# Kernel tuning notes

Measured on AMD Instinct MI355X. Metric: run time of the kernel, lower is better.

## Reference

```python
import jax, jax.numpy as jnp
import numpy as np

C = 256
NUM_GROUPS = 32
EPS = 1e-5


def group_norm(x, gamma, beta):
    # x: [B, C, H, W]; normalize within each of NUM_GROUPS channel groups
    B, Cc, H, W = x.shape
    xg = x.reshape(B, NUM_GROUPS, Cc // NUM_GROUPS, H, W)
    mean = xg.mean(axis=(2, 3, 4), keepdims=True)
    var = xg.var(axis=(2, 3, 4), keepdims=True)
    xg = (xg - mean) * jax.lax.rsqrt(var + EPS)
    x = xg.reshape(B, Cc, H, W)
    return x * gamma[None, :, None, None] + beta[None, :, None, None]


def conv1x1(x, w, b):
    # w: [C_out, C_in], b: [C_out]; equivalent to nn.Conv2d(k=1)
    return jnp.einsum('oc,bchw->bohw', w, x) + b[None, :, None, None]


def setup_inputs() -> dict:
    key = jax.random.key(0)
    ks = jax.random.split(key, 12)
    B, H, W = 8, 64, 64
    x = jax.random.normal(ks[0], (B, C, H, W), dtype=jnp.float32)
    temb = jax.random.normal(ks[1], (B, 512), dtype=jnp.float32)
    s = 1.0 / np.sqrt(C)  # kaiming-uniform-ish scale for 1x1 conv
    def wmat(k):
        return jax.random.uniform(k, (C, C), dtype=jnp.float32, minval=-s, maxval=s)
    def bvec(k):
        return jax.random.uniform(k, (C,), dtype=jnp.float32, minval=-s, maxval=s)
    return {
        'x': x, 'temb': temb,
        'gn_w': jnp.ones((C,), jnp.float32), 'gn_b': jnp.zeros((C,), jnp.float32),
        'wq': wmat(ks[2]), 'bq': bvec(ks[3]),
        'wk': wmat(ks[4]), 'bk': bvec(ks[5]),
        'wv': wmat(ks[6]), 'bv': bvec(ks[7]),
        'wp': wmat(ks[8]), 'bp': bvec(ks[9]),
    }


def reference(x, temb, gn_w, gn_b, wq, bq, wk, bk, wv, bv, wp, bp):
    B, Cc, H, W = x.shape
    h = group_norm(x, gn_w, gn_b)
    q = conv1x1(h, wq, bq)
    k = conv1x1(h, wk, bk)
    v = conv1x1(h, wv, bv)
    # full self-attention over spatial positions: scores [B, H, W, H, W]
    scale = Cc ** (-0.5)
    w = jnp.einsum('bchw,bcij->bhwij', q, k) * scale
    w = jax.nn.softmax(w.reshape(B, H, W, H * W), axis=-1).reshape(B, H, W, H, W)
    h = jnp.einsum('bhwij,bcij->bchw', w, v)
    h = conv1x1(h, wp, bp)
    return (x + h, temb)
```

## Files before the change

kernel.cpp:

```cpp
#include <hip/hip_runtime.h>
#include <hip/hip_bf16.h>

#define B_ 8
#define C_ 256
#define S_ 4096
#define G_ 32
#define GC_ 8
#define EPS_ 1e-5f

typedef __attribute__((ext_vector_type(4))) float f32x4;
typedef __attribute__((ext_vector_type(8))) short bf16x8;
typedef __attribute__((ext_vector_type(4))) short bf16x4;
typedef __attribute__((ext_vector_type(4))) unsigned int u32x4;
typedef __attribute__((ext_vector_type(2))) unsigned int u32x2;

#define DI __device__ __forceinline__

DI unsigned short f2bf(float f) {
    union { float f; unsigned u; } v; v.f = f;
    unsigned r = v.u + 0x7fffu + ((v.u >> 16) & 1u);
    return (unsigned short)(r >> 16);
}

DI unsigned cvt_pk_bf16(float lo, float hi) {
    unsigned r;
    asm("v_cvt_pk_bf16_f32 %0, %1, %2" : "=v"(r) : "v"(lo), "v"(hi));
    return r;
}

__global__ __launch_bounds__(256) void k_gn_stats(const float* __restrict__ x,
                                                  float* __restrict__ stats) {
    int bg = blockIdx.x;
    const float4* xp = (const float4*)(x + (size_t)bg * (GC_ * S_));
    float s = 0.f, ss = 0.f;
    for (int i = threadIdx.x; i < GC_ * S_ / 4; i += 256) {
        float4 v = xp[i];
        s  += v.x + v.y + v.z + v.w;
        ss += v.x * v.x + v.y * v.y + v.z * v.z + v.w * v.w;
    }
    #pragma unroll
    for (int off = 32; off; off >>= 1) { s += __shfl_down(s, off); ss += __shfl_down(ss, off); }
    __shared__ float rs[4], rss[4];
    int w = threadIdx.x >> 6;
    if ((threadIdx.x & 63) == 0) { rs[w] = s; rss[w] = ss; }
    __syncthreads();
    if (threadIdx.x == 0) {
        float S1 = rs[0] + rs[1] + rs[2] + rs[3];
        float S2 = rss[0] + rss[1] + rss[2] + rss[3];
        float inv = 1.f / (GC_ * S_);
        float mean = S1 * inv;
        float var = S2 * inv - mean * mean;
        stats[bg * 2] = mean;
        stats[bg * 2 + 1] = rsqrtf(var + EPS_);
    }
}

__global__ __launch_bounds__(256) void k_gn_apply(const float* __restrict__ x,
                                                  const float* __restrict__ stats,
                                                  const float* __restrict__ gw,
                                                  const float* __restrict__ gb,
                                                  unsigned short* __restrict__ h) {
    int b = blockIdx.x >> 6;
    int s0 = (blockIdx.x & 63) * 64;
    __shared__ unsigned short tile[64 * 256];
    const float* xb = x + (size_t)b * C_ * S_;
    for (int id = threadIdx.x; id < 256 * 16; id += 256) {
        int c = id >> 4, s4 = id & 15;
        float4 v = *(const float4*)(xb + (size_t)c * S_ + s0 + s4 * 4);
        float mean = stats[(b * G_ + (c >> 3)) * 2];
        float rstd = stats[(b * G_ + (c >> 3)) * 2 + 1];
        float ga = gw[c], be = gb[c];
        float vv[4] = {v.x, v.y, v.z, v.w};
        #pragma unroll
        for (int i = 0; i < 4; i++) {
            int srow = s4 * 4 + i;
            unsigned byte = srow * 512u + c * 2u;
            byte ^= ((srow & 7u) << 4);
            *(unsigned short*)((char*)tile + byte) = f2bf((vv[i] - mean) * rstd * ga + be);
        }
    }
    __syncthreads();
    unsigned short* hb = h + (size_t)b * S_ * C_;
    for (int id = threadIdx.x; id < 2048; id += 256) {
        int srow = id >> 5, ck = id & 31;
        unsigned byte = srow * 512u + ck * 16u;
        byte ^= ((srow & 7u) << 4);
        u32x4 v = *(u32x4*)((char*)tile + byte);
        *(u32x4*)(hb + (size_t)(s0 + srow) * C_ + ck * 8) = v;
    }
}

__global__ __launch_bounds__(256) void k_wcvt(const float* __restrict__ wq, const float* __restrict__ wk,
                                              const float* __restrict__ wv, const float* __restrict__ wp,
                                              unsigned short* __restrict__ wbf) {
    int t = blockIdx.x * 256 + threadIdx.x;
    int mat = t >> 13;
    int idx = (t & 8191) * 8;
    const float* src = mat == 0 ? wq : mat == 1 ? wk : mat == 2 ? wv : wp;
    float4 a = *(const float4*)(src + idx);
    float4 c = *(const float4*)(src + idx + 4);
    unsigned short tmp[8] = {f2bf(a.x), f2bf(a.y), f2bf(a.z), f2bf(a.w),
                             f2bf(c.x), f2bf(c.y), f2bf(c.z), f2bf(c.w)};
    *(u32x4*)(wbf + mat * 65536 + idx) = *(u32x4*)tmp;
}

__global__ __launch_bounds__(256) void k_qkv(const unsigned short* __restrict__ wbf,
                                             const float* __restrict__ bq,
                                             const float* __restrict__ bk,
                                             const float* __restrict__ bv,
                                             const unsigned short* __restrict__ h,
                                             unsigned short* __restrict__ q_sc,
                                             unsigned short* __restrict__ k_sc,
                                             unsigned short* __restrict__ v_cs,
                                             float qscale) {
    int mode = blockIdx.x >> 9;
    int inner = blockIdx.x & 511;
    int b = inner & 7;
    int rest = inner >> 3;
    int m0 = (rest & 1) * 128;
    int n0 = (rest >> 1) * 128;
    const unsigned short* W = wbf + mode * 65536;
    const float* bias = mode == 0 ? bq : (mode == 1 ? bk : bv);

    __shared__ unsigned short Alds[128 * 64];
    __shared__ unsigned short Blds[128 * 64];
    int tid = threadIdx.x;
    int lane = tid & 63, wv = tid >> 6;
    int wm = (wv >> 1) * 64, wn = (wv & 1) * 64;
    int lr = lane & 15, lg = lane >> 4;
    f32x4 acc[4][4] = {};
    const unsigned short* Bb = h + (size_t)b * S_ * C_;

    for (int k0 = 0; k0 < 256; k0 += 64) {
        __syncthreads();
        #pragma unroll
        for (int i = 0; i < 4; i++) {
            int id = tid + i * 256;
            int row = id >> 3, ck = id & 7;
            u32x4 v = *(const u32x4*)(W + (size_t)(m0 + row) * C_ + k0 + ck * 8);
            unsigned byte = row * 128u + ck * 16u;
            byte ^= ((row & 7u) << 4);
            *(u32x4*)((char*)Alds + byte) = v;
        }
        #pragma unroll
        for (int i = 0; i < 4; i++) {
            int id = tid + i * 256;
            int row = id >> 3, ck = id & 7;
            u32x4 v = *(const u32x4*)(Bb + (size_t)(n0 + row) * C_ + k0 + ck * 8);
            unsigned byte = row * 128u + ck * 16u;
            byte ^= ((row & 7u) << 4);
            *(u32x4*)((char*)Blds + byte) = v;
        }
        __syncthreads();
        #pragma unroll
        for (int ks = 0; ks < 2; ks++) {
            bf16x8 af[4], bf[4];
            #pragma unroll
            for (int mf = 0; mf < 4; mf++) {
                int m = wm + mf * 16 + lr;
                unsigned byte = m * 128u + ks * 64u + lg * 16u;
                byte ^= ((m & 7u) << 4);
                af[mf] = *(bf16x8*)((char*)Alds + byte);
            }
            #pragma unroll
            for (int nf = 0; nf < 4; nf++) {
                int n = wn + nf * 16 + lr;
                unsigned byte = n * 128u + ks * 64u + lg * 16u;
                byte ^= ((n & 7u) << 4);
                bf[nf] = *(bf16x8*)((char*)Blds + byte);
            }
            #pragma unroll
            for (int mf = 0; mf < 4; mf++)
                #pragma unroll
                for (int nf = 0; nf < 4; nf++)
                    acc[mf][nf] = __builtin_amdgcn_mfma_f32_16x16x32_bf16(af[mf], bf[nf], acc[mf][nf], 0, 0, 0);
        }
    }

    if (mode < 2) {
        unsigned short* ob = (mode == 0 ? q_sc : k_sc) + (size_t)b * S_ * C_;
        float sc = mode == 0 ? qscale : 1.f;
        #pragma unroll
        for (int mf = 0; mf < 4; mf++)
            #pragma unroll
            for (int nf = 0; nf < 4; nf++) {
                int cbase = m0 + wm + mf * 16 + lg * 4;
                int srow = n0 + wn + nf * 16 + lr;
                bf16x4 pk;
                #pragma unroll
                for (int r = 0; r < 4; r++)
                    pk[r] = (short)f2bf((acc[mf][nf][r] + bias[cbase + r]) * sc);
                *(bf16x4*)(ob + (size_t)srow * C_ + cbase) = pk;
            }
    } else {
        unsigned short* ob = v_cs + (size_t)b * C_ * S_;
        #pragma unroll
        for (int mf = 0; mf < 4; mf++)
            #pragma unroll
            for (int nf = 0; nf < 4; nf++)
                #pragma unroll
                for (int r = 0; r < 4; r++) {
                    int c = m0 + wm + mf * 16 + lg * 4 + r;
                    int s = n0 + wn + nf * 16 + lr;
                    ob[(size_t)c * S_ + s] = f2bf(acc[mf][nf][r] + bias[c]);
                }
    }
}

__global__ __launch_bounds__(256) void k_proj(const unsigned short* __restrict__ wbf,
                                              const float* __restrict__ bias,
                                              const unsigned short* __restrict__ Bm,
                                              float* __restrict__ outf,
                                              const float* __restrict__ xres) {
    int b = blockIdx.x & 7;
    int rest = blockIdx.x >> 3;
    int m0 = (rest & 1) * 128;
    int n0 = (rest >> 1) * 128;
    const unsigned short* W = wbf + 3 * 65536;

    __shared__ unsigned short Alds[128 * 64];
    __shared__ unsigned short Blds[128 * 64];
    int tid = threadIdx.x;
    int lane = tid & 63, wv = tid >> 6;
    int wm = (wv >> 1) * 64, wn = (wv & 1) * 64;
    int lr = lane & 15, lg = lane >> 4;
    f32x4 acc[4][4] = {};
    const unsigned short* Bb = Bm + (size_t)b * S_ * C_;

    for (int k0 = 0; k0 < 256; k0 += 64) {
        __syncthreads();
        #pragma unroll
        for (int i = 0; i < 4; i++) {
            int id = tid + i * 256;
            int row = id >> 3, ck = id & 7;
            u32x4 v = *(const u32x4*)(W + (size_t)(m0 + row) * C_ + k0 + ck * 8);
            unsigned byte = row * 128u + ck * 16u;
            byte ^= ((row & 7u) << 4);
            *(u32x4*)((char*)Alds + byte) = v;
        }
        #pragma unroll
        for (int i = 0; i < 4; i++) {
            int id = tid + i * 256;
            int row = id >> 3, ck = id & 7;
            u32x4 v = *(const u32x4*)(Bb + (size_t)(n0 + row) * C_ + k0 + ck * 8);
            unsigned byte = row * 128u + ck * 16u;
            byte ^= ((row & 7u) << 4);
            *(u32x4*)((char*)Blds + byte) = v;
        }
        __syncthreads();
        #pragma unroll
        for (int ks = 0; ks < 2; ks++) {
            bf16x8 af[4], bf[4];
            #pragma unroll
            for (int mf = 0; mf < 4; mf++) {
                int m = wm + mf * 16 + lr;
                unsigned byte = m * 128u + ks * 64u + lg * 16u;
                byte ^= ((m & 7u) << 4);
                af[mf] = *(bf16x8*)((char*)Alds + byte);
            }
            #pragma unroll
            for (int nf = 0; nf < 4; nf++) {
                int n = wn + nf * 16 + lr;
                unsigned byte = n * 128u + ks * 64u + lg * 16u;
                byte ^= ((n & 7u) << 4);
                bf[nf] = *(bf16x8*)((char*)Blds + byte);
            }
            #pragma unroll
            for (int mf = 0; mf < 4; mf++)
                #pragma unroll
                for (int nf = 0; nf < 4; nf++)
                    acc[mf][nf] = __builtin_amdgcn_mfma_f32_16x16x32_bf16(af[mf], bf[nf], acc[mf][nf], 0, 0, 0);
        }
    }

    const float* xb = xres + (size_t)b * C_ * S_;
    #pragma unroll
    for (int mf = 0; mf < 4; mf++)
        #pragma unroll
        for (int nf = 0; nf < 4; nf++)
            #pragma unroll
            for (int r = 0; r < 4; r++) {
                int c = m0 + wm + mf * 16 + lg * 4 + r;
                int s = n0 + wn + nf * 16 + lr;
                outf[(size_t)b * C_ * S_ + (size_t)c * S_ + s] =
                    acc[mf][nf][r] + bias[c] + xb[(size_t)c * S_ + s];
            }
}

__global__ __launch_bounds__(512, 2) void k_attn(const unsigned short* __restrict__ Q,
                                                 const unsigned short* __restrict__ K,
                                                 const unsigned short* __restrict__ V,
                                                 unsigned short* __restrict__ O) {
    int b = blockIdx.x & 7;
    int q0 = (blockIdx.x >> 3) * 128;
    int tid = threadIdx.x, lane = tid & 63, wv = tid >> 6;
    int lr = lane & 15, lg = lane >> 4;
    int qg = wv & 3, kg = wv >> 2;
    int qw = q0 + qg * 32;
    __shared__ unsigned short Klds[64 * 256];
    __shared__ unsigned short Vlds[256 * 64];
    __shared__ unsigned short Plds[4][32 * 64];
    __shared__ float mlp[8 * 2 * 16];
    const unsigned short* Qb = Q + (size_t)b * S_ * C_;
    const unsigned short* Kb = K + (size_t)b * S_ * C_;
    const unsigned short* Vb = V + (size_t)b * C_ * S_;

    bf16x8 qf_[8][2];
    #pragma unroll
    for (int ks = 0; ks < 8; ks++)
        #pragma unroll
        for (int qf = 0; qf < 2; qf++)
            qf_[ks][qf] = *(const bf16x8*)(Qb + (size_t)(qw + qf * 16 + lr) * C_ + ks * 32 + lg * 8);

    unsigned kaddr[2][8];
    #pragma unroll
    for (int kf = 0; kf < 2; kf++) {
        int key = kg * 32 + kf * 16 + lr;
        #pragma unroll
        for (int ks = 0; ks < 8; ks++)
            kaddr[kf][ks] = (unsigned)key * 512u + (((unsigned)(4 * ks + lg + 2 * key) & 31u) << 4);
    }

    f32x4 acc[8][2] = {};
    float lrun[2] = {0.f, 0.f};

    int krow[4], kck[4], vc[4], vck[4];
    #pragma unroll
    for (int i = 0; i < 4; i++) {
        int id = tid + i * 512;
        krow[i] = id >> 5; kck[i] = id & 31;
        vc[i] = id >> 3;  vck[i] = id & 7;
    }
    unsigned kwb[4], vwb[4];
    #pragma unroll
    for (int i = 0; i < 4; i++) {
        kwb[i] = krow[i] * 512u + (((unsigned)(kck[i] + 2 * krow[i]) & 31u) << 4);
        vwb[i] = vc[i] * 128u + ((vck[i] * 16u) ^ ((vc[i] & 7u) << 4));
    }

    u32x4 kpre[4], vpre[4];
    #pragma unroll
    for (int i = 0; i < 4; i++) {
        kpre[i] = *(const u32x4*)(Kb + (size_t)krow[i] * C_ + kck[i] * 8);
        vpre[i] = *(const u32x4*)(Vb + (size_t)vc[i] * S_ + vck[i] * 8);
    }
    #pragma unroll
    for (int i = 0; i < 4; i++) {
        *(u32x4*)((char*)Klds + kwb[i]) = kpre[i];
        *(u32x4*)((char*)Vlds + vwb[i]) = vpre[i];
    }
    __syncthreads();

    for (int kt = 0; kt < 64; kt++) {
        bool pf = (kt + 1) < 64;
        if (pf) {
            #pragma unroll
            for (int i = 0; i < 4; i++)
                kpre[i] = *(const u32x4*)(Kb + (size_t)((kt + 1) * 64 + krow[i]) * C_ + kck[i] * 8);
        }

        f32x4 sc[2][2] = {};
        #pragma unroll
        for (int ks = 0; ks < 8; ks++) {
            bf16x8 a[2];
            a[0] = *(const bf16x8*)((char*)Klds + kaddr[0][ks]);
            a[1] = *(const bf16x8*)((char*)Klds + kaddr[1][ks]);
            #pragma unroll
            for (int kf = 0; kf < 2; kf++)
                #pragma unroll
                for (int qf = 0; qf < 2; qf++)
                    sc[kf][qf] = __builtin_amdgcn_mfma_f32_16x16x32_bf16(a[kf], qf_[ks][qf], sc[kf][qf], 0, 0, 0);
        }

        #pragma unroll
        for (int qf = 0; qf < 2; qf++)
            #pragma unroll
            for (int kf = 0; kf < 2; kf++) {
                float p0 = __builtin_amdgcn_exp2f(sc[kf][qf][0] - 16.f);
                float p1 = __builtin_amdgcn_exp2f(sc[kf][qf][1] - 16.f);
                float p2 = __builtin_amdgcn_exp2f(sc[kf][qf][2] - 16.f);
                float p3 = __builtin_amdgcn_exp2f(sc[kf][qf][3] - 16.f);
                lrun[qf] += (p0 + p1) + (p2 + p3);
                u32x2 pk;
                pk[0] = cvt_pk_bf16(p0, p1);
                pk[1] = cvt_pk_bf16(p2, p3);
                int q = qf * 16 + lr;
                unsigned byte = (unsigned)q * 128u + (kg * 32u + kf * 16u + lg * 4u) * 2u;
                byte ^= ((q & 7u) << 4);
                *(u32x2*)((char*)&Plds[qg][0] + byte) = pk;
            }

        if (pf) {
            #pragma unroll
            for (int i = 0; i < 4; i++)
                vpre[i] = *(const u32x4*)(Vb + (size_t)vc[i] * S_ + (kt + 1) * 64 + vck[i] * 8);
        }

        __syncthreads();

        if (pf) {
            #pragma unroll
            for (int i = 0; i < 4; i++)
                *(u32x4*)((char*)Klds + kwb[i]) = kpre[i];
        }

        #pragma unroll
        for (int ks2 = 0; ks2 < 2; ks2++) {
            bf16x8 pb[2];
            #pragma unroll
            for (int qf = 0; qf < 2; qf++) {
                int q = qf * 16 + lr;
                unsigned pbyte = (unsigned)q * 128u + ks2 * 64u + lg * 16u;
                pbyte ^= ((q & 7u) << 4);
                pb[qf] = *(const bf16x8*)((char*)&Plds[qg][0] + pbyte);
            }
            #pragma unroll
            for (int cf = 0; cf < 8; cf++) {
                int c = kg * 128 + cf * 16 + lr;
                unsigned byte = c * 128u + ks2 * 64u + lg * 16u;
                byte ^= ((c & 7u) << 4);
                bf16x8 va = *(const bf16x8*)((char*)Vlds + byte);
                #pragma unroll
                for (int qf = 0; qf < 2; qf++)
                    acc[cf][qf] = __builtin_amdgcn_mfma_f32_16x16x32_bf16(va, pb[qf], acc[cf][qf], 0, 0, 0);
            }
        }

        __syncthreads();

        if (pf) {
            #pragma unroll
            for (int i = 0; i < 4; i++)
                *(u32x4*)((char*)Vlds + vwb[i]) = vpre[i];
        }
    }

    float ls[2];
    #pragma unroll
    for (int qf = 0; qf < 2; qf++) {
        float t = lrun[qf];
        t += __shfl_xor(t, 16);
        t += __shfl_xor(t, 32);
        ls[qf] = t;
    }
    if (lg == 0) {
        #pragma unroll
        for (int qf = 0; qf < 2; qf++) mlp[(wv * 2 + qf) * 16 + lr] = ls[qf];
    }
    __syncthreads();
    unsigned short* Ob = O + (size_t)b * S_ * C_;
    #pragma unroll
    for (int qf = 0; qf < 2; qf++) {
        float inv = 1.f / (ls[qf] + mlp[((wv ^ 4) * 2 + qf) * 16 + lr]);
        int srow = qw + qf * 16 + lr;
        #pragma unroll
        for (int cf = 0; cf < 8; cf++) {
            u32x2 pk;
            pk[0] = cvt_pk_bf16(acc[cf][qf][0] * inv, acc[cf][qf][1] * inv);
            pk[1] = cvt_pk_bf16(acc[cf][qf][2] * inv, acc[cf][qf][3] * inv);
            *(u32x2*)(Ob + (size_t)srow * C_ + kg * 128 + cf * 16 + lg * 4) = pk;
        }
    }
}

__global__ __launch_bounds__(256) void k_copy_temb(const float* __restrict__ t, float* __restrict__ o) {
    int i = blockIdx.x * 256 + threadIdx.x;
    if (i < B_ * 512) o[i] = t[i];
}

extern "C" void kernel_launch(void* const* d_in, const int* in_sizes, int n_in,
                              void* d_out, int out_size, void* d_ws, size_t ws_size,
                              hipStream_t stream) {
    (void)in_sizes; (void)n_in; (void)out_size; (void)ws_size;
    const float* x  = (const float*)d_in[0];
    const float* temb = (const float*)d_in[1];
    const float* gw = (const float*)d_in[2];
    const float* gb = (const float*)d_in[3];
    const float* wq = (const float*)d_in[4];
    const float* bq = (const float*)d_in[5];
    const float* wk = (const float*)d_in[6];
    const float* bk = (const float*)d_in[7];
    const float* wv = (const float*)d_in[8];
    const float* bv = (const float*)d_in[9];
    const float* wp = (const float*)d_in[10];
    const float* bp = (const float*)d_in[11];
    float* out = (float*)d_out;

    char* ws = (char*)d_ws;
    const size_t MB16 = (size_t)B_ * S_ * C_ * 2;
    unsigned short* h_sc = (unsigned short*)ws;
    unsigned short* q_sc = (unsigned short*)(ws + MB16);
    unsigned short* k_sc = (unsigned short*)(ws + 2 * MB16);
    unsigned short* v_cs = (unsigned short*)(ws + 3 * MB16);
    float* stats = (float*)(ws + 4 * MB16);
    unsigned short* wbf = (unsigned short*)(ws + 4 * MB16 + 4096);

    const float qscale = 0.0625f * 1.4426950408889634f;

    k_wcvt<<<128, 256, 0, stream>>>(wq, wk, wv, wp, wbf);
    k_gn_stats<<<B_ * G_, 256, 0, stream>>>(x, stats);
    k_gn_apply<<<B_ * (S_ / 64), 256, 0, stream>>>(x, stats, gw, gb, h_sc);
    k_qkv<<<1536, 256, 0, stream>>>(wbf, bq, bk, bv, h_sc, q_sc, k_sc, v_cs, qscale);
    k_attn<<<B_ * (S_ / 128), 512, 0, stream>>>(q_sc, k_sc, v_cs, h_sc);
    k_proj<<<512, 256, 0, stream>>>(wbf, bp, h_sc, out, x);
    k_copy_temb<<<(B_ * 512 + 255) / 256, 256, 0, stream>>>(temb, out + (size_t)B_ * C_ * S_);
}
```

Before: 213.7 us.

## Store Q and K in FP8 and compute attention scores with FP8 MFMA

The QKV kernel now writes Q and K as unscaled FP8 (e4m3) instead of pre-scaled bf16. The attention kernel loads these into half-size LDS tiles and computes QK^T with FP8 16x16x32 MFMA, folding the softmax scale into an fma before exp2. This halves Q/K memory traffic and LDS footprint and raises score matmul throughput, at the cost of reduced precision in the attention scores. Softmax still uses a fixed max offset of 16 with no running max, so the lower precision may affect accuracy.

Result: faster. 196.9 us (-7.8%).

```diff
diff --git a/kernel.cpp b/kernel.cpp
--- a/kernel.cpp
+++ b/kernel.cpp
@@ -26,6 +26,18 @@
     unsigned r;
     asm("v_cvt_pk_bf16_f32 %0, %1, %2" : "=v"(r) : "v"(lo), "v"(hi));
     return r;
+}
+
+DI unsigned cvt_pk_fp8(float lo, float hi) {
+    unsigned r;
+    asm("v_cvt_pk_fp8_f32 %0, %1, %2" : "=v"(r) : "v"(lo), "v"(hi));
+    return r;
+}
+
+DI f32x4 mfma_fp8(u32x2 a, u32x2 b, f32x4 c) {
+    union { u32x2 u; long l; } ua, ub;
+    ua.u = a; ub.u = b;
+    return __builtin_amdgcn_mfma_f32_16x16x32_fp8_fp8(ua.l, ub.l, c, 0, 0, 0);
 }
 
 __global__ __launch_bounds__(256) void k_gn_stats(const float* __restrict__ x,
@@ -109,10 +121,9 @@
                                              const float* __restrict__ bk,
                                              const float* __restrict__ bv,
                                              const unsigned short* __restrict__ h,
-                                             unsigned short* __restrict__ q_sc,
-                                             unsigned short* __restrict__ k_sc,
-                                             unsigned short* __restrict__ v_cs,
-                                             float qscale) {
+                                             unsigned char* __restrict__ q8,
+                                             unsigned char* __restrict__ k8,
+                                             unsigned short* __restrict__ v_cs) {
     int mode = blockIdx.x >> 9;
     int inner = blockIdx.x & 511;
     int b = inner & 7;
@@ -178,19 +189,20 @@
     }
 
     if (mode < 2) {
-        unsigned short* ob = (mode == 0 ? q_sc : k_sc) + (size_t)b * S_ * C_;
-        float sc = mode == 0 ? qscale : 1.f;
+        unsigned char* ob = (mode == 0 ? q8 : k8) + (size_t)b * S_ * C_;
         #pragma unroll
         for (int mf = 0; mf < 4; mf++)
             #pragma unroll
             for (int nf = 0; nf < 4; nf++) {
                 int cbase = m0 + wm + mf * 16 + lg * 4;
                 int srow = n0 + wn + nf * 16 + lr;
-                bf16x4 pk;
-                #pragma unroll
-                for (int r = 0; r < 4; r++)
-                    pk[r] = (short)f2bf((acc[mf][nf][r] + bias[cbase + r]) * sc);
-                *(bf16x4*)(ob + (size_t)srow * C_ + cbase) = pk;
+                float v0 = acc[mf][nf][0] + bias[cbase + 0];
+                float v1 = acc[mf][nf][1] + bias[cbase + 1];
+                float v2 = acc[mf][nf][2] + bias[cbase + 2];
+                float v3 = acc[mf][nf][3] + bias[cbase + 3];
+                unsigned lo = cvt_pk_fp8(v0, v1);
+                unsigned hi = cvt_pk_fp8(v2, v3);
+                *(unsigned*)(ob + (size_t)srow * C_ + cbase) = (lo & 0xffffu) | (hi << 16);
             }
     } else {
         unsigned short* ob = v_cs + (size_t)b * C_ * S_;
@@ -287,8 +299,8 @@
             }
 }
 
-__global__ __launch_bounds__(512, 2) void k_attn(const unsigned short* __restrict__ Q,
-                                                 const unsigned short* __restrict__ K,
+__global__ __launch_bounds__(512, 2) void k_attn(const unsigned char* __restrict__ Q8,
+                                                 const unsigned char* __restrict__ K8,
                                                  const unsigned short* __restrict__ V,
                                                  unsigned short* __restrict__ O) {
     int b = blockIdx.x & 7;
@@ -297,20 +309,22 @@
     int lr = lane & 15, lg = lane >> 4;
     int qg = wv & 3, kg = wv >> 2;
     int qw = q0 + qg * 32;
-    __shared__ unsigned short Klds[64 * 256];
+    __shared__ unsigned char  Klds8[64 * 256];
     __shared__ unsigned short Vlds[256 * 64];
     __shared__ unsigned short Plds[4][32 * 64];
     __shared__ float mlp[8 * 2 * 16];
-    const unsigned short* Qb = Q + (size_t)b * S_ * C_;
-    const unsigned short* Kb = K + (size_t)b * S_ * C_;
+    const unsigned char*  Qb = Q8 + (size_t)b * S_ * C_;
+    const unsigned char*  Kb = K8 + (size_t)b * S_ * C_;
     const unsigned short* Vb = V + (size_t)b * C_ * S_;
 
-    bf16x8 qf_[8][2];
+    const float QS = 0.09016844f;
+
+    u32x2 qf8[8][2];
     #pragma unroll
     for (int ks = 0; ks < 8; ks++)
         #pragma unroll
         for (int qf = 0; qf < 2; qf++)
-            qf_[ks][qf] = *(const bf16x8*)(Qb + (size_t)(qw + qf * 16 + lr) * C_ + ks * 32 + lg * 8);
+            qf8[ks][qf] = *(const u32x2*)(Qb + (size_t)(qw + qf * 16 + lr) * C_ + ks * 32 + lg * 8);
 
     unsigned kaddr[2][8];
     #pragma unroll
@@ -318,68 +332,73 @@
         int key = kg * 32 + kf * 16 + lr;
         #pragma unroll
         for (int ks = 0; ks < 8; ks++)
-            kaddr[kf][ks] = (unsigned)key * 512u + (((unsigned)(4 * ks + lg + 2 * key) & 31u) << 4);
+            kaddr[kf][ks] = (unsigned)key * 256u + (((unsigned)(4 * ks + lg + 2 * key) & 31u) << 3);
     }
 
     f32x4 acc[8][2] = {};
     float lrun[2] = {0.f, 0.f};
 
-    int krow[4], kck[4], vc[4], vck[4];
+    int kr0[2], kc16[2], vc[4], vck[4];
+    #pragma unroll
+    for (int i = 0; i < 2; i++) {
+        int id = tid + i * 512;
+        kr0[i] = id >> 4; kc16[i] = id & 15;
+    }
     #pragma unroll
     for (int i = 0; i < 4; i++) {
         int id = tid + i * 512;
-        krow[i] = id >> 5; kck[i] = id & 31;
         vc[i] = id >> 3;  vck[i] = id & 7;
     }
-    unsigned kwb[4], vwb[4];
-    #pragma unroll
-    for (int i = 0; i < 4; i++) {
-        kwb[i] = krow[i] * 512u + (((unsigned)(kck[i] + 2 * krow[i]) & 31u) << 4);
+    unsigned kwb[2], vwb[4];
+    #pragma unroll
+    for (int i = 0; i < 2; i++)
+        kwb[i] = kr0[i] * 256u + (((unsigned)(2 * kc16[i] + 2 * kr0[i]) & 31u) << 3);
+    #pragma unroll
+    for (int i = 0; i < 4; i++)
         vwb[i] = vc[i] * 128u + ((vck[i] * 16u) ^ ((vc[i] & 7u) << 4));
-    }
-
-    u32x4 kpre[4], vpre[4];
-    #pragma unroll
-    for (int i = 0; i < 4; i++) {
-        kpre[i] = *(const u32x4*)(Kb + (size_t)krow[i] * C_ + kck[i] * 8);
+
+    u32x4 kpre[2], vpre[4];
+    #pragma unroll
+    for (int i = 0; i < 2; i++)
+        kpre[i] = *(const u32x4*)(Kb + (size_t)kr0[i] * C_ + kc16[i] * 16);
+    #pragma unroll
+    for (int i = 0; i < 4; i++)
         vpre[i] = *(const u32x4*)(Vb + (size_t)vc[i] * S_ + vck[i] * 8);
-    }
-    #pragma unroll
-    for (int i = 0; i < 4; i++) {
-        *(u32x4*)((char*)Klds + kwb[i]) = kpre[i];
+    #pragma unroll
+    for (int i = 0; i < 2; i++)
+        *(u32x4*)(Klds8 + kwb[i]) = kpre[i];
+    #pragma unroll
+    for (int i = 0; i < 4; i++)
         *(u32x4*)((char*)Vlds + vwb[i]) = vpre[i];
-    }
     __syncthreads();
 
     for (int kt = 0; kt < 64; kt++) {
         bool pf = (kt + 1) < 64;
         if (pf) {
             #pragma unroll
-            for (int i = 0; i < 4; i++)
-                kpre[i] = *(const u32x4*)(Kb + (size_t)((kt + 1) * 64 + krow[i]) * C_ + kck[i] * 8);
+            for (int i = 0; i < 2; i++)
+                kpre[i] = *(const u32x4*)(Kb + (size_t)((kt + 1) * 64 + kr0[i]) * C_ + kc16[i] * 16);
         }
 
         f32x4 sc[2][2] = {};
         #pragma unroll
         for (int ks = 0; ks < 8; ks++) {
-            bf16x8 a[2];
-            a[0] = *(const bf16x8*)((char*)Klds + kaddr[0][ks]);
-            a[1] = *(const bf16x8*)((char*)Klds + kaddr[1][ks]);
-            #pragma unroll
-            for (int kf = 0; kf < 2; kf++)
-                #pragma unroll
-                for (int qf = 0; qf < 2; qf++)
-                    sc[kf][qf] = __builtin_amdgcn_mfma_f32_16x16x32_bf16(a[kf], qf_[ks][qf], sc[kf][qf], 0, 0, 0);
+            u32x2 a0 = *(const u32x2*)(Klds8 + kaddr[0][ks]);
+            u32x2 a1 = *(const u32x2*)(Klds8 + kaddr[1][ks]);
+            sc[0][0] = mfma_fp8(a0, qf8[ks][0], sc[0][0]);
+            sc[0][1] = mfma_fp8(a0, qf8[ks][1], sc[0][1]);
+            sc[1][0] = mfma_fp8(a1, qf8[ks][0], sc[1][0]);
+            sc[1][1] = mfma_fp8(a1, qf8[ks][1], sc[1][1]);
         }
 
         #pragma unroll
         for (int qf = 0; qf < 2; qf++)
             #pragma unroll
             for (int kf = 0; kf < 2; kf++) {
-                float p0 = __builtin_amdgcn_exp2f(sc[kf][qf][0] - 16.f);
-                float p1 = __builtin_amdgcn_exp2f(sc[kf][qf][1] - 16.f);
-                float p2 = __builtin_amdgcn_exp2f(sc[kf][qf][2] - 16.f);
-                float p3 = __builtin_amdgcn_exp2f(sc[kf][qf][3] - 16.f);
+                float p0 = __builtin_amdgcn_exp2f(fmaf(sc[kf][qf][0], QS, -16.f));
+                float p1 = __builtin_amdgcn_exp2f(fmaf(sc[kf][qf][1], QS, -16.f));
+                float p2 = __builtin_amdgcn_exp2f(fmaf(sc[kf][qf][2], QS, -16.f));
+                float p3 = __builtin_amdgcn_exp2f(fmaf(sc[kf][qf][3], QS, -16.f));
                 lrun[qf] += (p0 + p1) + (p2 + p3);
                 u32x2 pk;
                 pk[0] = cvt_pk_bf16(p0, p1);
@@ -400,8 +419,8 @@
 
         if (pf) {
             #pragma unroll
-            for (int i = 0; i < 4; i++)
-                *(u32x4*)((char*)Klds + kwb[i]) = kpre[i];
+            for (int i = 0; i < 2; i++)
+                *(u32x4*)(Klds8 + kwb[i]) = kpre[i];
         }
 
         #pragma unroll
@@ -487,21 +506,19 @@
     float* out = (float*)d_out;
 
     char* ws = (char*)d_ws;
-    const size_t MB16 = (size_t)B_ * S_ * C_ * 2;
+    const size_t MB = 1024 * 1024;
     unsigned short* h_sc = (unsigned short*)ws;
-    unsigned short* q_sc = (unsigned short*)(ws + MB16);
-    unsigned short* k_sc = (unsigned short*)(ws + 2 * MB16);
-    unsigned short* v_cs = (unsigned short*)(ws + 3 * MB16);
-    float* stats = (float*)(ws + 4 * MB16);
-    unsigned short* wbf = (unsigned short*)(ws + 4 * MB16 + 4096);
-
-    const float qscale = 0.0625f * 1.4426950408889634f;
+    unsigned short* v_cs = (unsigned short*)(ws + 16 * MB);
+    unsigned char*  q8   = (unsigned char*)(ws + 32 * MB);
+    unsigned char*  k8   = (unsigned char*)(ws + 40 * MB);
+    float* stats = (float*)(ws + 48 * MB);
+    unsigned short* wbf = (unsigned short*)(ws + 48 * MB + 4096);
 
     k_wcvt<<<128, 256, 0, stream>>>(wq, wk, wv, wp, wbf);
     k_gn_stats<<<B_ * G_, 256, 0, stream>>>(x, stats);
     k_gn_apply<<<B_ * (S_ / 64), 256, 0, stream>>>(x, stats, gw, gb, h_sc);
-    k_qkv<<<1536, 256, 0, stream>>>(wbf, bq, bk, bv, h_sc, q_sc, k_sc, v_cs, qscale);
-    k_attn<<<B_ * (S_ / 128), 512, 0, stream>>>(q_sc, k_sc, v_cs, h_sc);
+    k_qkv<<<1536, 256, 0, stream>>>(wbf, bq, bk, bv, h_sc, q8, k8, v_cs);
+    k_attn<<<B_ * (S_ / 128), 512, 0, stream>>>(q8, k8, v_cs, h_sc);
     k_proj<<<512, 256, 0, stream>>>(wbf, bp, h_sc, out, x);
     k_copy_temb<<<(B_ * 512 + 255) / 256, 256, 0, stream>>>(temb, out + (size_t)B_ * C_ * S_);
 }
```
